# Kernel optimization log

Measured on AMD Instinct MI355X. Metric: run time of the kernel, lower is better.

The kernel has to match this reference:

```python
import jax, jax.numpy as jnp
import numpy as np

N_NODES = 50000
N_GRAPHS = 64
NEG_SLOPE = 0.2


def gat_conv(x, src, dst, W, a_src, a_dst, b, n_nodes, concat):
    """PyG-style GATConv (eval mode, self-loops already in src/dst).
    x: [N, Fin], W: [Fin, H*C], a_src/a_dst: [H, C], b: [H*C] or [C].
    """
    H, C = a_src.shape
    h = (x @ W).reshape(n_nodes, H, C)                      # [N,H,C]
    al_src = jnp.einsum('nhc,hc->nh', h, a_src)             # [N,H]
    al_dst = jnp.einsum('nhc,hc->nh', h, a_dst)             # [N,H]
    e = jax.nn.leaky_relu(al_src[src] + al_dst[dst], NEG_SLOPE)  # [E,H]
    # softmax over incoming edges per destination node
    m = jax.ops.segment_max(e, dst, num_segments=n_nodes)   # [N,H]
    ex = jnp.exp(e - m[dst])
    s = jax.ops.segment_sum(ex, dst, num_segments=n_nodes)  # [N,H]
    alpha = ex / (s[dst] + 1e-16)                           # [E,H]
    # attention-weighted aggregation of source features
    out = jax.ops.segment_sum(h[src] * alpha[..., None], dst, num_segments=n_nodes)  # [N,H,C]
    out = out.reshape(n_nodes, H * C) if concat else out.mean(axis=1)
    return out + b


def setup_inputs() -> dict:
    key = jax.random.key(0)
    ks = jax.random.split(key, 12)
    n, e = N_NODES, 800000
    x = jax.random.normal(ks[0], (n, 500), dtype=jnp.float32)
    edge_index = jax.random.randint(ks[1], (2, e), 0, n, dtype=jnp.int64)
    batch = jnp.sort(jax.random.randint(ks[2], (n,), 0, N_GRAPHS, dtype=jnp.int64))
    hid, heads = 64, 4
    sc = 0.1
    W1 = jax.random.normal(ks[3], (500, heads * hid), dtype=jnp.float32) * sc
    a_src1 = jax.random.normal(ks[4], (heads, hid), dtype=jnp.float32) * sc
    a_dst1 = jax.random.normal(ks[5], (heads, hid), dtype=jnp.float32) * sc
    b1 = jnp.zeros((heads * hid,), dtype=jnp.float32)
    W2 = jax.random.normal(ks[6], (heads * hid, hid), dtype=jnp.float32) * sc
    a_src2 = jax.random.normal(ks[7], (1, hid), dtype=jnp.float32) * sc
    a_dst2 = jax.random.normal(ks[8], (1, hid), dtype=jnp.float32) * sc
    b2 = jnp.zeros((hid,), dtype=jnp.float32)
    Wl = jax.random.normal(ks[9], (hid, 2), dtype=jnp.float32) * sc
    bl = jnp.zeros((2,), dtype=jnp.float32)
    return dict(x=x, edge_index=edge_index, batch=batch,
                W1=W1, a_src1=a_src1, a_dst1=a_dst1, b1=b1,
                W2=W2, a_src2=a_src2, a_dst2=a_dst2, b2=b2,
                Wl=Wl, bl=bl)


def reference(x, edge_index, batch, W1, a_src1, a_dst1, b1,
              W2, a_src2, a_dst2, b2, Wl, bl):
    n = x.shape[0]
    # PyG GATConv adds self-loops by default
    loops = jnp.arange(n, dtype=edge_index.dtype)
    src = jnp.concatenate([edge_index[0], loops])
    dst = jnp.concatenate([edge_index[1], loops])
    h = jax.nn.relu(gat_conv(x, src, dst, W1, a_src1, a_dst1, b1, n, concat=True))
    h = jax.nn.relu(gat_conv(h, src, dst, W2, a_src2, a_dst2, b2, n, concat=False))
    # global mean pool over graphs
    sums = jax.ops.segment_sum(h, batch, num_segments=N_GRAPHS)      # [G, hid]
    cnt = jax.ops.segment_sum(jnp.ones((n,), h.dtype), batch, num_segments=N_GRAPHS)
    pooled = sums / jnp.maximum(cnt, 1.0)[:, None]
    return pooled @ Wl + bl                                          # [G, 2]
```

## Files before the change

kernel.cpp:

```cpp
#include <hip/hip_runtime.h>
#include <math.h>

#define NN   50000
#define NE   800000
#define NET  850000
#define NG   64
#define KIN  500
#define NEG  0.2f

typedef unsigned short ushort_t;
typedef __attribute__((ext_vector_type(8))) short bf8_t;
typedef __attribute__((ext_vector_type(8))) unsigned short us8_t;
typedef __attribute__((ext_vector_type(4))) float f4_t;
typedef __attribute__((ext_vector_type(2))) float f2_t;
typedef __attribute__((ext_vector_type(4))) unsigned u4_t;
typedef __attribute__((ext_vector_type(2))) unsigned u2_t;

__device__ __forceinline__ float bf2f(ushort_t u) {
    unsigned v = ((unsigned)u) << 16;
    return __builtin_bit_cast(float, v);
}
__device__ __forceinline__ ushort_t f2bf(float f) {
    unsigned b = __builtin_bit_cast(unsigned, f);
    unsigned r = (b + 0x7FFFu + ((b >> 16) & 1u)) >> 16;
    return (ushort_t)r;
}

#if __has_builtin(__builtin_amdgcn_cvt_f32_fp8)
#define FP8DEC(w, b) __builtin_amdgcn_cvt_f32_fp8((w), (b))
#else
__device__ __forceinline__ float fp8_sw_dec(unsigned w, int b) {
    unsigned by = (w >> (8 * b)) & 0xFFu;
    unsigned s = by >> 7, e = (by >> 3) & 15u, m = by & 7u;
    float v = e ? __builtin_bit_cast(float, ((e + 120u) << 23) | (m << 20))
                : (float)m * 0.001953125f;
    return s ? -v : v;
}
#define FP8DEC(w, b) fp8_sw_dec((w), (b))
#endif

#if __has_builtin(__builtin_amdgcn_cvt_pk_f32_fp8)
__device__ __forceinline__ f2_t fp8_pk_lo(unsigned w) {
    return __builtin_amdgcn_cvt_pk_f32_fp8(w, false);
}
__device__ __forceinline__ f2_t fp8_pk_hi(unsigned w) {
    return __builtin_amdgcn_cvt_pk_f32_fp8(w, true);
}
#else
__device__ __forceinline__ f2_t fp8_pk_lo(unsigned w) {
    f2_t r; r.x = FP8DEC(w, 0); r.y = FP8DEC(w, 1); return r;
}
__device__ __forceinline__ f2_t fp8_pk_hi(unsigned w) {
    f2_t r; r.x = FP8DEC(w, 2); r.y = FP8DEC(w, 3); return r;
}
#endif

#if __has_builtin(__builtin_amdgcn_cvt_pk_fp8_f32)
__device__ __forceinline__ unsigned char f2fp8(float f) {
    return (unsigned char)(__builtin_amdgcn_cvt_pk_fp8_f32(f, 0.f, 0u, false) & 0xFFu);
}
#else
__device__ __forceinline__ unsigned char f2fp8(float f) {
    unsigned u = __builtin_bit_cast(unsigned, f);
    unsigned sgn = (u >> 24) & 0x80u;
    float a = fabsf(f);
    if (!(a < 448.f)) return (unsigned char)(sgn | 0x7Eu);
    if (a < 0.015625f) {
        int m = (int)(a * 512.f + 0.5f);
        return (unsigned char)(sgn | (m > 7 ? 8 : m));
    }
    unsigned r = u + 0x7FFFFu + ((u >> 20) & 1u);
    unsigned e = (r >> 23) & 0xFFu;
    unsigned m = (r >> 20) & 7u;
    if (e > 135u) return (unsigned char)(sgn | 0x7Eu);
    return (unsigned char)(sgn | ((e - 120u) << 3) | m);
}
#endif

#define GLOAD_LDS(g, l)                                                        \
    __builtin_amdgcn_global_load_lds(                                          \
        (const __attribute__((address_space(1))) unsigned int*)(g),            \
        (__attribute__((address_space(3))) unsigned int*)(l), 16, 0, 0)

__global__ void k_deg(const int* __restrict__ ei, int* __restrict__ deg) {
    int e = blockIdx.x * 256 + threadIdx.x;
    if (e >= NET) return;
    int dst = (e < NE) ? ei[NE + e] : (e - NE);
    atomicAdd(&deg[dst], 1);
}

__global__ void k_scan_part(const int* __restrict__ deg, int* __restrict__ part) {
    __shared__ int s[256];
    int t = threadIdx.x;
    int i = blockIdx.x * 256 + t;
    s[t] = (i < NN) ? deg[i] : 0;
    __syncthreads();
    for (int off = 128; off > 0; off >>= 1) {
        if (t < off) s[t] += s[t + off];
        __syncthreads();
    }
    if (t == 0) part[blockIdx.x] = s[0];
}

__global__ void k_scan_top(int* __restrict__ part, int nb) {
    __shared__ int s[256];
    int t = threadIdx.x;
    int v = (t < nb) ? part[t] : 0;
    s[t] = v;
    __syncthreads();
    for (int off = 1; off < 256; off <<= 1) {
        int a = (t >= off) ? s[t - off] : 0;
        __syncthreads();
        s[t] += a;
        __syncthreads();
    }
    if (t < nb) part[t] = s[t] - v;
}

__global__ void k_scan_apply(const int* __restrict__ deg, const int* __restrict__ part,
                             int* __restrict__ rowptr) {
    __shared__ int s[256];
    int t = threadIdx.x;
    int i = blockIdx.x * 256 + t;
    int v = (i < NN) ? deg[i] : 0;
    s[t] = v;
    __syncthreads();
    for (int off = 1; off < 256; off <<= 1) {
        int a = (t >= off) ? s[t - off] : 0;
        __syncthreads();
        s[t] += a;
        __syncthreads();
    }
    if (i < NN) rowptr[i] = part[blockIdx.x] + s[t] - v;
    if (i == 0) rowptr[NN] = NET;
}

__global__ void k_fill(const int* __restrict__ ei, const int* __restrict__ rowptr,
                       int* __restrict__ cursor, int* __restrict__ csr) {
    int e = blockIdx.x * 256 + threadIdx.x;
    if (e >= NET) return;
    int src, dst;
    if (e < NE) { src = ei[e]; dst = ei[NE + e]; }
    else        { src = dst = e - NE; }
    int pos = atomicAdd(&cursor[dst], 1);
    csr[rowptr[dst] + pos] = src;
}

template <int KSRC, int KPAD, int NOUT>
__global__ void k_cast_wt(const float* __restrict__ W, ushort_t* __restrict__ Wt) {
    int idx = blockIdx.x * 256 + threadIdx.x;
    if (idx >= NOUT * KPAD) return;
    int n = idx / KPAD, k = idx - n * KPAD;
    float v = (k < KSRC) ? W[(size_t)k * NOUT + n] : 0.f;
    Wt[idx] = f2bf(v);
}

__global__ __launch_bounds__(512) void k_mfma1f(
    const float* __restrict__ x, const ushort_t* __restrict__ Wt,
    const float* __restrict__ a_s, const float* __restrict__ a_d,
    unsigned char* __restrict__ Hb, float* __restrict__ als, float* __restrict__ ald)
{
    __shared__ __align__(16) ushort_t lA[128 * 32];
    __shared__ __align__(16) ushort_t lB[256 * 32];
    const int t    = threadIdx.x;
    const int row0 = blockIdx.y * 128;
    const int ww   = t >> 6, lane = t & 63;
    const int wm   = ww & 1, wn = ww >> 1;
    const int lrow = lane & 15, lq = lane >> 4;

    const int arow  = t >> 2;
    const int akq   = t & 3;
    const int arowg = row0 + arow;
    const bool arok = arowg < NN;
    const float* xrow = x + (size_t)arowg * KIN;

    f4_t acc[4][4] = {};

    for (int k0 = 0; k0 < 512; k0 += 32) {
        int kk = k0 + akq * 8;
        float4 v0 = make_float4(0.f, 0.f, 0.f, 0.f);
        float4 v1 = make_float4(0.f, 0.f, 0.f, 0.f);
        if (arok && kk + 4 <= KIN) {
            v0 = *(const float4*)(xrow + kk);
            if (kk + 8 <= KIN) v1 = *(const float4*)(xrow + kk + 4);
        }
        us8_t ab;
        ab[0] = f2bf(v0.x); ab[1] = f2bf(v0.y); ab[2] = f2bf(v0.z); ab[3] = f2bf(v0.w);
        ab[4] = f2bf(v1.x); ab[5] = f2bf(v1.y); ab[6] = f2bf(v1.z); ab[7] = f2bf(v1.w);
        *(us8_t*)&lA[arow * 32 + akq * 8] = ab;
#pragma unroll
        for (int i = 0; i < 2; i++) {
            int c = i * 512 + t;
            int row = c >> 2, kq = c & 3;
            const ushort_t* gp = Wt + (size_t)row * 512 + k0 + kq * 8;
            GLOAD_LDS(gp, &lB[c * 8]);
        }
        __syncthreads();
        bf8_t af[4], bfr[4];
#pragma unroll
        for (int i = 0; i < 4; i++)
            af[i] = *(const bf8_t*)&lA[(wm * 64 + i * 16 + lrow) * 32 + lq * 8];
#pragma unroll
        for (int j = 0; j < 4; j++)
            bfr[j] = *(const bf8_t*)&lB[(wn * 64 + j * 16 + lrow) * 32 + lq * 8];
#pragma unroll
        for (int i = 0; i < 4; i++)
#pragma unroll
            for (int j = 0; j < 4; j++)
                acc[i][j] = __builtin_amdgcn_mfma_f32_16x16x32_bf16(af[i], bfr[j], acc[i][j], 0, 0, 0);
        __syncthreads();
    }

    const int head = wn;
    float as4[4], ad4[4];
#pragma unroll
    for (int j = 0; j < 4; j++) {
        as4[j] = a_s[head * 64 + j * 16 + lrow];
        ad4[j] = a_d[head * 64 + j * 16 + lrow];
    }
#pragma unroll
    for (int i = 0; i < 4; i++) {
#pragma unroll
        for (int r = 0; r < 4; r++) {
            int row = row0 + wm * 64 + i * 16 + lq * 4 + r;
            float v0 = acc[i][0][r], v1 = acc[i][1][r], v2 = acc[i][2][r], v3 = acc[i][3][r];
            if (row < NN) {
                size_t base = (size_t)row * 256 + wn * 64 + lrow;
                Hb[base +  0] = f2fp8(v0);
                Hb[base + 16] = f2fp8(v1);
                Hb[base + 32] = f2fp8(v2);
                Hb[base + 48] = f2fp8(v3);
            }
            float ps = v0 * as4[0] + v1 * as4[1] + v2 * as4[2] + v3 * as4[3];
            float pd = v0 * ad4[0] + v1 * ad4[1] + v2 * ad4[2] + v3 * ad4[3];
#pragma unroll
            for (int off = 1; off < 16; off <<= 1) {
                ps += __shfl_xor(ps, off);
                pd += __shfl_xor(pd, off);
            }
            if (lrow == 0 && row < NN) {
                als[(size_t)row * 4 + head] = ps;
                ald[(size_t)row * 4 + head] = pd;
            }
        }
    }
}

template <int K, int LDA, int BM, int BN, int WM, int FOUT, int HEADS>
__global__ __launch_bounds__(256) void k_mfma(
    const ushort_t* __restrict__ A, const ushort_t* __restrict__ Wt,
    const float* __restrict__ a_s, const float* __restrict__ a_d,
    unsigned char* __restrict__ Hb, float* __restrict__ als, float* __restrict__ ald)
{
    __shared__ __align__(16) ushort_t lA[BM * 32];
    __shared__ __align__(16) ushort_t lB[BN * 32];
    const int t    = threadIdx.x;
    const int row0 = blockIdx.y * BM;
    const int n0   = blockIdx.x * BN;
    const int ww   = t >> 6, lane = t & 63;
    const int wm   = ww % WM, wn = ww / WM;
    const int lrow = lane & 15, lq = lane >> 4;

    f4_t acc[4][4] = {};

    for (int k0 = 0; k0 < K; k0 += 32) {
#pragma unroll
        for (int i = 0; i < BM / 64; i++) {
            int c = i * 256 + t;
            int row = c >> 2, kq = c & 3;
            const ushort_t* gp = A + (size_t)(row0 + row) * LDA + k0 + kq * 8;
            GLOAD_LDS(gp, &lA[c * 8]);
        }
#pragma unroll
        for (int i = 0; i < BN / 64; i++) {
            int c = i * 256 + t;
            int row = c >> 2, kq = c & 3;
            const ushort_t* gp = Wt + (size_t)(n0 + row) * K + k0 + kq * 8;
            GLOAD_LDS(gp, &lB[c * 8]);
        }
        __syncthreads();
        bf8_t af[4], bfr[4];
#pragma unroll
        for (int i = 0; i < 4; i++)
            af[i] = *(const bf8_t*)&lA[(wm * 64 + i * 16 + lrow) * 32 + lq * 8];
#pragma unroll
        for (int j = 0; j < 4; j++)
            bfr[j] = *(const bf8_t*)&lB[(wn * 64 + j * 16 + lrow) * 32 + lq * 8];
#pragma unroll
        for (int i = 0; i < 4; i++)
#pragma unroll
            for (int j = 0; j < 4; j++)
                acc[i][j] = __builtin_amdgcn_mfma_f32_16x16x32_bf16(af[i], bfr[j], acc[i][j], 0, 0, 0);
        __syncthreads();
    }

    const int head = (n0 + wn * 64) >> 6;
    float as4[4], ad4[4];
#pragma unroll
    for (int j = 0; j < 4; j++) {
        as4[j] = a_s[head * 64 + j * 16 + lrow];
        ad4[j] = a_d[head * 64 + j * 16 + lrow];
    }
#pragma unroll
    for (int i = 0; i < 4; i++) {
#pragma unroll
        for (int r = 0; r < 4; r++) {
            int row = row0 + wm * 64 + i * 16 + lq * 4 + r;
            float v0 = acc[i][0][r], v1 = acc[i][1][r], v2 = acc[i][2][r], v3 = acc[i][3][r];
            if (row < NN) {
                size_t base = (size_t)row * FOUT + n0 + wn * 64 + lrow;
                Hb[base +  0] = f2fp8(v0);
                Hb[base + 16] = f2fp8(v1);
                Hb[base + 32] = f2fp8(v2);
                Hb[base + 48] = f2fp8(v3);
            }
            float ps = v0 * as4[0] + v1 * as4[1] + v2 * as4[2] + v3 * as4[3];
            float pd = v0 * ad4[0] + v1 * ad4[1] + v2 * ad4[2] + v3 * ad4[3];
#pragma unroll
            for (int off = 1; off < 16; off <<= 1) {
                ps += __shfl_xor(ps, off);
                pd += __shfl_xor(pd, off);
            }
            if (lrow == 0 && row < NN) {
                als[(size_t)row * HEADS + head] = ps;
                ald[(size_t)row * HEADS + head] = pd;
            }
        }
    }
}

#define CAP1 128
__global__ __launch_bounds__(256) void k_agg1(
    const int* __restrict__ rowptr, const int* __restrict__ csr,
    const unsigned char* __restrict__ Hb, const float* __restrict__ als,
    const float* __restrict__ ald, const float* __restrict__ bias,
    ushort_t* __restrict__ OutB)
{
    __shared__ float salpha[4][CAP1 * 4];
    int w = threadIdx.x >> 6, lane = threadIdx.x & 63;
    int dst = blockIdx.x * 4 + w;
    if (dst >= NN) return;
    float* Aw = salpha[w];
    const int beg = rowptr[dst], end = rowptr[dst + 1];
    const int deg = end - beg;

    const int hd    = lane & 3;
    const int slot  = lane >> 2;
    const int slot2 = lane >> 4;
    const int head2 = (lane >> 2) & 3;
    const int f0    = (lane & 3) * 16;

    int  ke    = slot2;
    bool valid = ke < deg;
    int  src   = csr[beg + (valid ? ke : 0)];
    u4_t xv    = *(const u4_t*)&Hb[(size_t)src * 256 + head2 * 64 + f0];

    const float adst = ald[dst * 4 + hd];
    float m = -1e30f, s = 0.f;
    for (int k = slot; k < deg; k += 16) {
        int sk = csr[beg + k];
        float e = als[sk * 4 + hd] + adst;
        e = (e > 0.f) ? e : NEG * e;
        if (k < CAP1) Aw[k * 4 + hd] = e;
        float mn = fmaxf(m, e);
        s = s * __expf(m - mn) + __expf(e - mn);
        m = mn;
    }
#pragma unroll
    for (int off = 4; off < 64; off <<= 1) {
        float mo = __shfl_xor(m, off);
        float so = __shfl_xor(s, off);
        float mn = fmaxf(m, mo);
        s = s * __expf(m - mn) + so * __expf(mo - mn);
        m = mn;
    }
    float inv = 1.f / (s + 1e-16f);
    int cap4 = (deg < CAP1 ? deg : CAP1) * 4;
    for (int j = lane; j < cap4; j += 64)
        Aw[j] = __expf(Aw[j] - m) * inv;

    const float m2  = __shfl(m, head2);
    const float i2  = __shfl(inv, head2);
    const float ad2 = __shfl(adst, head2);

    f2_t facc2[8] = {};
    int k0 = 0;
    while (true) {
        int k0n = k0 + 4;
        bool more = k0n < deg;
        int srcn = 0; u4_t xvn = {}; bool validn = false;
        if (more) {
            int ken = k0n + slot2;
            validn = ken < deg;
            srcn = csr[beg + (validn ? ken : 0)];
            xvn  = *(const u4_t*)&Hb[(size_t)srcn * 256 + head2 * 64 + f0];
        }
        float al = 0.f;
        if (valid) {
            if (ke < CAP1) {
                al = Aw[ke * 4 + head2];
            } else {
                float e = als[src * 4 + head2] + ad2;
                e = (e > 0.f) ? e : NEG * e;
                al = __expf(e - m2) * i2;
            }
        }
        f2_t al2; al2.x = al; al2.y = al;
#pragma unroll
        for (int wd = 0; wd < 4; wd++) {
            unsigned wv = xv[wd];
            facc2[wd * 2 + 0] += al2 * fp8_pk_lo(wv);
            facc2[wd * 2 + 1] += al2 * fp8_pk_hi(wv);
        }
        if (!more) break;
        k0 = k0n; ke = k0 + slot2; valid = validn; src = srcn; xv = xvn;
    }
    float facc[16];
#pragma unroll
    for (int j = 0; j < 8; j++) { facc[j * 2] = facc2[j].x; facc[j * 2 + 1] = facc2[j].y; }
#pragma unroll
    for (int j = 0; j < 16; j++) {
        facc[j] += __shfl_xor(facc[j], 16);
        facc[j] += __shfl_xor(facc[j], 32);
    }
    if (lane < 16) {
        us8_t oa, ob;
#pragma unroll
        for (int j = 0; j < 8; j++) {
            float o  = facc[j]     + bias[head2 * 64 + f0 + j];
            float o2 = facc[8 + j] + bias[head2 * 64 + f0 + 8 + j];
            oa[j] = f2bf(o  > 0.f ? o  : 0.f);
            ob[j] = f2bf(o2 > 0.f ? o2 : 0.f);
        }
        *(us8_t*)&OutB[(size_t)dst * 256 + head2 * 64 + f0]     = oa;
        *(us8_t*)&OutB[(size_t)dst * 256 + head2 * 64 + f0 + 8] = ob;
    }
}

#define CAP2 128
__global__ __launch_bounds__(256) void k_agg2(
    const int* __restrict__ rowptr, const int* __restrict__ csr,
    const unsigned char* __restrict__ Hb, const float* __restrict__ als,
    const float* __restrict__ ald, const float* __restrict__ bias,
    float* __restrict__ OutF)
{
    __shared__ float salpha2[4][CAP2];
    int w = threadIdx.x >> 6, lane = threadIdx.x & 63;
    int dst = blockIdx.x * 4 + w;
    if (dst >= NN) return;
    float* Aw = salpha2[w];
    const int beg = rowptr[dst], end = rowptr[dst + 1];
    const int deg = end - beg;
    const float adst = ald[dst];

    const int slot2 = lane >> 3;
    const int f0    = (lane & 7) * 8;

    int  ke    = slot2;
    bool valid = ke < deg;
    int  src   = csr[beg + (valid ? ke : 0)];
    u2_t xv    = *(const u2_t*)&Hb[(size_t)src * 64 + f0];

    float m = -1e30f, s = 0.f;
    for (int k = lane; k < deg; k += 64) {
        int sk = csr[beg + k];
        float e = als[sk] + adst;
        e = (e > 0.f) ? e : NEG * e;
        if (k < CAP2) Aw[k] = e;
        float mn = fmaxf(m, e);
        s = s * __expf(m - mn) + __expf(e - mn);
        m = mn;
    }
#pragma unroll
    for (int off = 1; off < 64; off <<= 1) {
        float mo = __shfl_xor(m, off);
        float so = __shfl_xor(s, off);
        float mn = fmaxf(m, mo);
        s = s * __expf(m - mn) + so * __expf(mo - mn);
        m = mn;
    }
    float inv = 1.f / (s + 1e-16f);
    int cap = deg < CAP2 ? deg : CAP2;
    for (int j = lane; j < cap; j += 64)
        Aw[j] = __expf(Aw[j] - m) * inv;

    f2_t facc2[4] = {};
    int k0 = 0;
    while (true) {
        int k0n = k0 + 8;
        bool more = k0n < deg;
        int srcn = 0; u2_t xvn = {}; bool validn = false;
        if (more) {
            int ken = k0n + slot2;
            validn = ken < deg;
            srcn = csr[beg + (validn ? ken : 0)];
            xvn  = *(const u2_t*)&Hb[(size_t)srcn * 64 + f0];
        }
        float al = 0.f;
        if (valid) {
            if (ke < CAP2) {
                al = Aw[ke];
            } else {
                float e = als[src] + adst;
                e = (e > 0.f) ? e : NEG * e;
                al = __expf(e - m) * inv;
            }
        }
        f2_t al2; al2.x = al; al2.y = al;
#pragma unroll
        for (int wd = 0; wd < 2; wd++) {
            unsigned wv = xv[wd];
            facc2[wd * 2 + 0] += al2 * fp8_pk_lo(wv);
            facc2[wd * 2 + 1] += al2 * fp8_pk_hi(wv);
        }
        if (!more) break;
        k0 = k0n; ke = k0 + slot2; valid = validn; src = srcn; xv = xvn;
    }
    float facc[8];
#pragma unroll
    for (int j = 0; j < 4; j++) { facc[j * 2] = facc2[j].x; facc[j * 2 + 1] = facc2[j].y; }
#pragma unroll
    for (int j = 0; j < 8; j++) {
        facc[j] += __shfl_xor(facc[j], 8);
        facc[j] += __shfl_xor(facc[j], 16);
        facc[j] += __shfl_xor(facc[j], 32);
    }
    if (lane < 8) {
        float4 oa, ob;
        float* pa = &oa.x; float* pb = &ob.x;
#pragma unroll
        for (int j = 0; j < 4; j++) {
            float v  = facc[j]     + bias[f0 + j];
            float v2 = facc[4 + j] + bias[f0 + 4 + j];
            pa[j] = (v  > 0.f) ? v  : 0.f;
            pb[j] = (v2 > 0.f) ? v2 : 0.f;
        }
        *(float4*)&OutF[(size_t)dst * 64 + f0]     = oa;
        *(float4*)&OutF[(size_t)dst * 64 + f0 + 4] = ob;
    }
}

#define PSPLIT 8
__global__ __launch_bounds__(256) void k_pool_part(
    const float* __restrict__ out2, const int* __restrict__ batch,
    float* __restrict__ pooled)
{
    int g = blockIdx.x >> 3, sp = blockIdx.x & 7;
    int lo, hi;
    { int a = 0, b = NN; while (a < b) { int mm = (a + b) >> 1; if (batch[mm] < g) a = mm + 1; else b = mm; } lo = a; }
    { int a = lo, b = NN; while (a < b) { int mm = (a + b) >> 1; if (batch[mm] < g + 1) a = mm + 1; else b = mm; } hi = a; }
    int t = threadIdx.x, c = t & 63, r = t >> 6;
    float s = 0.f;
    for (int n = lo + sp * 4 + r; n < hi; n += 32)
        s += out2[(size_t)n * 64 + c];
    __shared__ float red[256];
    red[t] = s;
    __syncthreads();
    if (t < 64) {
        float p = red[t] + red[t + 64] + red[t + 128] + red[t + 192];
        atomicAdd(&pooled[g * 64 + t], p);
    }
}

__global__ void k_final(const float* __restrict__ pooled, const int* __restrict__ batch,
                        const float* __restrict__ Wl, const float* __restrict__ bl,
                        float* __restrict__ out)
{
    int g = blockIdx.x;
    int lo, hi;
    { int a = 0, b = NN; while (a < b) { int mm = (a + b) >> 1; if (batch[mm] < g) a = mm + 1; else b = mm; } lo = a; }
    { int a = lo, b = NN; while (a < b) { int mm = (a + b) >> 1; if (batch[mm] < g + 1) a = mm + 1; else b = mm; } hi = a; }
    int t = threadIdx.x;
    int cnt = hi - lo;
    float p = pooled[g * 64 + t] / (float)(cnt > 0 ? cnt : 1);
    float r0 = p * Wl[t * 2 + 0];
    float r1 = p * Wl[t * 2 + 1];
#pragma unroll
    for (int off = 32; off > 0; off >>= 1) {
        r0 += __shfl_xor(r0, off);
        r1 += __shfl_xor(r1, off);
    }
    if (t == 0) {
        out[g * 2 + 0] = r0 + bl[0];
        out[g * 2 + 1] = r1 + bl[1];
    }
}

extern "C" void kernel_launch(void* const* d_in, const int* in_sizes, int n_in,
                              void* d_out, int out_size, void* d_ws, size_t ws_size,
                              hipStream_t stream)
{
    const float* x    = (const float*)d_in[0];
    const int*   ei   = (const int*)  d_in[1];
    const int*   batch= (const int*)  d_in[2];
    const float* W1   = (const float*)d_in[3];
    const float* as1  = (const float*)d_in[4];
    const float* ad1  = (const float*)d_in[5];
    const float* b1   = (const float*)d_in[6];
    const float* W2   = (const float*)d_in[7];
    const float* as2  = (const float*)d_in[8];
    const float* ad2  = (const float*)d_in[9];
    const float* b2   = (const float*)d_in[10];
    const float* Wl   = (const float*)d_in[11];
    const float* bl   = (const float*)d_in[12];
    float* out = (float*)d_out;

    int*   deg    = (int*)d_ws;
    int*   cursor = deg + 50048;
    int*   part   = cursor + 50048;
    int*   rowptr = part + 256;
    int*   csr    = rowptr + 50064;
    ushort_t* xb  = (ushort_t*)(csr + 850048);
    ushort_t* Wt1 = xb + (size_t)50048 * 512;
    ushort_t* Wt2 = Wt1 + 131072;
    ushort_t* h1b = Wt2 + 16384;
    unsigned char* h1b8 = (unsigned char*)h1b;
    float* al1s   = (float*)(h1b + (size_t)50000 * 256);
    float* al1d   = al1s + 200000;
    float* al2s   = al1d + 200000;
    float* al2d   = al2s + 50000;
    float* pooled = al2d + 50000;
    ushort_t* out1b = xb;
    unsigned char* h2b8 = (unsigned char*)(xb + 13000000);
    float*    out2  = (float*)(xb + 16400000);

    hipMemsetAsync(deg, 0, 2 * 50048 * sizeof(int), stream);
    hipMemsetAsync(pooled, 0, NG * 64 * sizeof(float), stream);

    k_deg       <<<(NET + 255) / 256, 256, 0, stream>>>(ei, deg);
    k_scan_part <<<196, 256, 0, stream>>>(deg, part);
    k_scan_top  <<<1,   256, 0, stream>>>(part, 196);
    k_scan_apply<<<196, 256, 0, stream>>>(deg, part, rowptr);
    k_fill      <<<(NET + 255) / 256, 256, 0, stream>>>(ei, rowptr, cursor, csr);

    k_cast_wt<500, 512, 256><<<(256 * 512 + 255) / 256, 256, 0, stream>>>(W1, Wt1);
    k_cast_wt<256, 256, 64> <<<(64 * 256 + 255) / 256, 256, 0, stream>>>(W2, Wt2);

    k_mfma1f<<<dim3(1, 391), 512, 0, stream>>>(x, Wt1, as1, ad1, h1b8, al1s, al1d);
    k_agg1<<<(NN + 3) / 4, 256, 0, stream>>>(rowptr, csr, h1b8, al1s, al1d, b1, out1b);
    hipMemsetAsync(out1b + (size_t)50000 * 256, 0, (size_t)176 * 256 * sizeof(ushort_t), stream);

    k_mfma<256, 256, 256, 64, 4, 64, 1><<<dim3(1, 196), 256, 0, stream>>>(
        out1b, Wt2, as2, ad2, h2b8, al2s, al2d);
    k_agg2<<<(NN + 3) / 4, 256, 0, stream>>>(rowptr, csr, h2b8, al2s, al2d, b2, out2);

    k_pool_part<<<NG * PSPLIT, 256, 0, stream>>>(out2, batch, pooled);
    k_final    <<<NG, 64, 0, stream>>>(pooled, batch, Wl, bl, out);
}
```

Measured before the change: 419.0 us.

## Double-buffer LDS tiles in layer-1 MFMA GEMM and pad A rows

Result: no change. 423.3 us (+1.0%).

```diff
diff --git a/kernel.cpp b/kernel.cpp
--- a/kernel.cpp
+++ b/kernel.cpp
@@ -155,13 +155,14 @@
     Wt[idx] = f2bf(v);
 }
 
+#define LDA_PAD 40
 __global__ __launch_bounds__(512) void k_mfma1f(
     const float* __restrict__ x, const ushort_t* __restrict__ Wt,
     const float* __restrict__ a_s, const float* __restrict__ a_d,
     unsigned char* __restrict__ Hb, float* __restrict__ als, float* __restrict__ ald)
 {
-    __shared__ __align__(16) ushort_t lA[128 * 32];
-    __shared__ __align__(16) ushort_t lB[256 * 32];
+    __shared__ __align__(16) ushort_t lA[2][128 * LDA_PAD];
+    __shared__ __align__(16) ushort_t lB[2][256 * 32];
     const int t    = threadIdx.x;
     const int row0 = blockIdx.y * 128;
     const int ww   = t >> 6, lane = t & 63;
@@ -176,39 +177,66 @@
 
     f4_t acc[4][4] = {};
 
-    for (int k0 = 0; k0 < 512; k0 += 32) {
-        int kk = k0 + akq * 8;
+    {
+        int kk = akq * 8;
         float4 v0 = make_float4(0.f, 0.f, 0.f, 0.f);
         float4 v1 = make_float4(0.f, 0.f, 0.f, 0.f);
-        if (arok && kk + 4 <= KIN) {
-            v0 = *(const float4*)(xrow + kk);
+        if (arok) {
+            if (kk + 4 <= KIN) v0 = *(const float4*)(xrow + kk);
             if (kk + 8 <= KIN) v1 = *(const float4*)(xrow + kk + 4);
+        }
+#pragma unroll
+        for (int i = 0; i < 2; i++) {
+            int c = i * 512 + t;
+            int row = c >> 2, kq = c & 3;
+            GLOAD_LDS(Wt + (size_t)row * 512 + kq * 8, &lB[0][c * 8]);
         }
         us8_t ab;
         ab[0] = f2bf(v0.x); ab[1] = f2bf(v0.y); ab[2] = f2bf(v0.z); ab[3] = f2bf(v0.w);
         ab[4] = f2bf(v1.x); ab[5] = f2bf(v1.y); ab[6] = f2bf(v1.z); ab[7] = f2bf(v1.w);
-        *(us8_t*)&lA[arow * 32 + akq * 8] = ab;
-#pragma unroll
-        for (int i = 0; i < 2; i++) {
-            int c = i * 512 + t;
-            int row = c >> 2, kq = c & 3;
-            const ushort_t* gp = Wt + (size_t)row * 512 + k0 + kq * 8;
-            GLOAD_LDS(gp, &lB[c * 8]);
-        }
-        __syncthreads();
+        *(us8_t*)&lA[0][arow * LDA_PAD + akq * 8] = ab;
+    }
+    __syncthreads();
+
+    int cur = 0;
+    for (int k0 = 0; k0 < 512; k0 += 32) {
+        const int kn = k0 + 32;
+        const bool more = kn < 512;
+        float4 p0 = make_float4(0.f, 0.f, 0.f, 0.f);
+        float4 p1 = make_float4(0.f, 0.f, 0.f, 0.f);
+        if (more) {
+            int kk = kn + akq * 8;
+            if (arok) {
+                if (kk + 4 <= KIN) p0 = *(const float4*)(xrow + kk);
+                if (kk + 8 <= KIN) p1 = *(const float4*)(xrow + kk + 4);
+            }
+#pragma unroll
+            for (int i = 0; i < 2; i++) {
+                int c = i * 512 + t;
+                int row = c >> 2, kq = c & 3;
+                GLOAD_LDS(Wt + (size_t)row * 512 + kn + kq * 8, &lB[cur ^ 1][c * 8]);
+            }
+        }
         bf8_t af[4], bfr[4];
 #pragma unroll
         for (int i = 0; i < 4; i++)
-            af[i] = *(const bf8_t*)&lA[(wm * 64 + i * 16 + lrow) * 32 + lq * 8];
+            af[i] = *(const bf8_t*)&lA[cur][(wm * 64 + i * 16 + lrow) * LDA_PAD + lq * 8];
 #pragma unroll
         for (int j = 0; j < 4; j++)
-            bfr[j] = *(const bf8_t*)&lB[(wn * 64 + j * 16 + lrow) * 32 + lq * 8];
+            bfr[j] = *(const bf8_t*)&lB[cur][(wn * 64 + j * 16 + lrow) * 32 + lq * 8];
 #pragma unroll
         for (int i = 0; i < 4; i++)
 #pragma unroll
             for (int j = 0; j < 4; j++)
                 acc[i][j] = __builtin_amdgcn_mfma_f32_16x16x32_bf16(af[i], bfr[j], acc[i][j], 0, 0, 0);
-        __syncthreads();
+        if (more) {
+            us8_t ab;
+            ab[0] = f2bf(p0.x); ab[1] = f2bf(p0.y); ab[2] = f2bf(p0.z); ab[3] = f2bf(p0.w);
+            ab[4] = f2bf(p1.x); ab[5] = f2bf(p1.y); ab[6] = f2bf(p1.z); ab[7] = f2bf(p1.w);
+            *(us8_t*)&lA[cur ^ 1][arow * LDA_PAD + akq * 8] = ab;
+        }
+        __syncthreads();
+        cur ^= 1;
     }
 
     const int head = wn;
```

## Split first-layer GEMM across two column blocks with 256-thread workgroups

Applied to the files above, without the earlier changes.

Result: slower. 452.7 us (+8.1%).

```diff
diff --git a/kernel.cpp b/kernel.cpp
--- a/kernel.cpp
+++ b/kernel.cpp
@@ -155,46 +155,55 @@
     Wt[idx] = f2bf(v);
 }
 
-__global__ __launch_bounds__(512) void k_mfma1f(
+__global__ __launch_bounds__(256) void k_mfma1f(
     const float* __restrict__ x, const ushort_t* __restrict__ Wt,
     const float* __restrict__ a_s, const float* __restrict__ a_d,
     unsigned char* __restrict__ Hb, float* __restrict__ als, float* __restrict__ ald)
 {
     __shared__ __align__(16) ushort_t lA[128 * 32];
-    __shared__ __align__(16) ushort_t lB[256 * 32];
+    __shared__ __align__(16) ushort_t lB[128 * 32];
     const int t    = threadIdx.x;
     const int row0 = blockIdx.y * 128;
+    const int n0   = blockIdx.x * 128;
     const int ww   = t >> 6, lane = t & 63;
     const int wm   = ww & 1, wn = ww >> 1;
     const int lrow = lane & 15, lq = lane >> 4;
 
-    const int arow  = t >> 2;
-    const int akq   = t & 3;
-    const int arowg = row0 + arow;
-    const bool arok = arowg < NN;
-    const float* xrow = x + (size_t)arowg * KIN;
+    const int ar0 = (t >> 2);
+    const int ar1 = (256 + t) >> 2;
+    const int akq = t & 3;
+    const bool aok0 = (row0 + ar0) < NN;
+    const bool aok1 = (row0 + ar1) < NN;
+    const float* xr0 = x + (size_t)(row0 + ar0) * KIN;
+    const float* xr1 = x + (size_t)(row0 + ar1) * KIN;
 
     f4_t acc[4][4] = {};
 
     for (int k0 = 0; k0 < 512; k0 += 32) {
         int kk = k0 + akq * 8;
-        float4 v0 = make_float4(0.f, 0.f, 0.f, 0.f);
-        float4 v1 = make_float4(0.f, 0.f, 0.f, 0.f);
-        if (arok && kk + 4 <= KIN) {
-            v0 = *(const float4*)(xrow + kk);
-            if (kk + 8 <= KIN) v1 = *(const float4*)(xrow + kk + 4);
-        }
-        us8_t ab;
-        ab[0] = f2bf(v0.x); ab[1] = f2bf(v0.y); ab[2] = f2bf(v0.z); ab[3] = f2bf(v0.w);
-        ab[4] = f2bf(v1.x); ab[5] = f2bf(v1.y); ab[6] = f2bf(v1.z); ab[7] = f2bf(v1.w);
-        *(us8_t*)&lA[arow * 32 + akq * 8] = ab;
+        float4 a00 = make_float4(0.f, 0.f, 0.f, 0.f), a01 = a00;
+        float4 a10 = a00, a11 = a00;
+        if (kk + 4 <= KIN) {
+            if (aok0) a00 = *(const float4*)(xr0 + kk);
+            if (aok1) a10 = *(const float4*)(xr1 + kk);
+            if (kk + 8 <= KIN) {
+                if (aok0) a01 = *(const float4*)(xr0 + kk + 4);
+                if (aok1) a11 = *(const float4*)(xr1 + kk + 4);
+            }
+        }
 #pragma unroll
         for (int i = 0; i < 2; i++) {
-            int c = i * 512 + t;
+            int c = i * 256 + t;
             int row = c >> 2, kq = c & 3;
-            const ushort_t* gp = Wt + (size_t)row * 512 + k0 + kq * 8;
-            GLOAD_LDS(gp, &lB[c * 8]);
-        }
+            GLOAD_LDS(Wt + (size_t)(n0 + row) * 512 + k0 + kq * 8, &lB[c * 8]);
+        }
+        us8_t ab0, ab1;
+        ab0[0] = f2bf(a00.x); ab0[1] = f2bf(a00.y); ab0[2] = f2bf(a00.z); ab0[3] = f2bf(a00.w);
+        ab0[4] = f2bf(a01.x); ab0[5] = f2bf(a01.y); ab0[6] = f2bf(a01.z); ab0[7] = f2bf(a01.w);
+        ab1[0] = f2bf(a10.x); ab1[1] = f2bf(a10.y); ab1[2] = f2bf(a10.z); ab1[3] = f2bf(a10.w);
+        ab1[4] = f2bf(a11.x); ab1[5] = f2bf(a11.y); ab1[6] = f2bf(a11.z); ab1[7] = f2bf(a11.w);
+        *(us8_t*)&lA[ar0 * 32 + akq * 8] = ab0;
+        *(us8_t*)&lA[ar1 * 32 + akq * 8] = ab1;
         __syncthreads();
         bf8_t af[4], bfr[4];
 #pragma unroll
@@ -211,7 +220,7 @@
         __syncthreads();
     }
 
-    const int head = wn;
+    const int head = (n0 + wn * 64) >> 6;
     float as4[4], ad4[4];
 #pragma unroll
     for (int j = 0; j < 4; j++) {
@@ -225,7 +234,7 @@
             int row = row0 + wm * 64 + i * 16 + lq * 4 + r;
             float v0 = acc[i][0][r], v1 = acc[i][1][r], v2 = acc[i][2][r], v3 = acc[i][3][r];
             if (row < NN) {
-                size_t base = (size_t)row * 256 + wn * 64 + lrow;
+                size_t base = (size_t)row * 256 + n0 + wn * 64 + lrow;
                 Hb[base +  0] = f2fp8(v0);
                 Hb[base + 16] = f2fp8(v1);
                 Hb[base + 32] = f2fp8(v2);
@@ -636,7 +645,7 @@
     k_cast_wt<500, 512, 256><<<(256 * 512 + 255) / 256, 256, 0, stream>>>(W1, Wt1);
     k_cast_wt<256, 256, 64> <<<(64 * 256 + 255) / 256, 256, 0, stream>>>(W2, Wt2);
 
-    k_mfma1f<<<dim3(1, 391), 512, 0, stream>>>(x, Wt1, as1, ad1, h1b8, al1s, al1d);
+    k_mfma1f<<<dim3(2, 391), 256, 0, stream>>>(x, Wt1, as1, ad1, h1b8, al1s, al1d);
     k_agg1<<<(NN + 3) / 4, 256, 0, stream>>>(rowptr, csr, h1b8, al1s, al1d, b1, out1b);
     hipMemsetAsync(out1b + (size_t)50000 * 256, 0, (size_t)176 * 256 * sizeof(ushort_t), stream);
 
```
